# Optimization experiments

Measured on AMD Instinct MI355X. Metric: run time of the kernel, lower is better.

Reference implementation:

```python
import jax, jax.numpy as jnp
import numpy as np

B, S, D, H = 2, 2048, 1024, 16
DK = D // H

def setup_inputs() -> dict:
    key = jax.random.key(0)
    ks = jax.random.split(key, 12)
    def lin(k):
        kw, kb = jax.random.split(k)
        bound = 1.0 / np.sqrt(D)
        W = jax.random.uniform(kw, (D, D), jnp.float32, -bound, bound)
        b = jax.random.uniform(kb, (D,), jnp.float32, -bound, bound)
        return W, b
    Wq, bq = lin(ks[0]); Wk, bk = lin(ks[1]); Wv, bv = lin(ks[2]); Wo, bo = lin(ks[3])
    q = jax.random.normal(ks[4], (B, S, D), jnp.float32)
    k = jax.random.normal(ks[5], (B, S, D), jnp.float32)
    v = jax.random.normal(ks[6], (B, S, D), jnp.float32)
    mask = jnp.ones((1, 1, S, S), jnp.int32)
    return {"q": q, "k": k, "v": v, "mask": mask,
            "Wq": Wq, "bq": bq, "Wk": Wk, "bk": bk,
            "Wv": Wv, "bv": bv, "Wo": Wo, "bo": bo}

def reference(q, k, v, mask, Wq, bq, Wk, bk, Wv, bv, Wo, bo):
    # torch Linear: y = x @ W.T + b
    Q = (q @ Wq.T + bq).reshape(B, S, H, DK).transpose(0, 2, 1, 3)  # [B,H,S,DK]
    K = (k @ Wk.T + bk).reshape(B, S, H, DK).transpose(0, 2, 1, 3)
    V = (v @ Wv.T + bv).reshape(B, S, H, DK).transpose(0, 2, 1, 3)
    scores = jnp.einsum('bhqd,bhkd->bhqk', Q, K) / jnp.sqrt(jnp.float32(DK))
    scores = jnp.where(mask == 0, jnp.float32(-1e9), scores)
    attn = jax.nn.softmax(scores, axis=-1)
    context = jnp.einsum('bhqk,bhkd->bhqd', attn, V)  # [B,H,S,DK]
    concat = context.transpose(0, 2, 1, 3).reshape(B, S, D)
    return concat @ Wo.T + bo
```

## Files before the change

### kernel.cpp

```cpp
#include <hip/hip_runtime.h>
#include <hip/hip_bf16.h>

#define BB 2
#define SS 2048
#define DD 1024
#define HH 16
#define DKK 64

typedef __hip_bfloat16 bf16;
typedef unsigned short u16;
using frag_ab = __attribute__((ext_vector_type(8))) short;
using frag_cd = __attribute__((ext_vector_type(4))) float;

__device__ inline u16 f2bf(float f) {
    bf16 h = __float2bfloat16(f);
    return *reinterpret_cast<u16*>(&h);
}

__device__ inline void gld16(const void* g, void* l) {
    __builtin_amdgcn_global_load_lds((const __attribute__((address_space(1))) void*)g,
                                     (__attribute__((address_space(3))) void*)l,
                                     16, 0, 0);
}

__global__ __launch_bounds__(256) void prep(
    const float* __restrict__ q, const float* __restrict__ k, const float* __restrict__ v,
    const float* __restrict__ Wq, const float* __restrict__ Wk,
    const float* __restrict__ Wv, const float* __restrict__ Wo,
    u16* __restrict__ qb, u16* __restrict__ kb, u16* __restrict__ vb,
    u16* __restrict__ Wqb, u16* __restrict__ Wkb, u16* __restrict__ Wvb, u16* __restrict__ Wob,
    const int* __restrict__ mask, int* __restrict__ flags) {
    int bid = blockIdx.x;
    int t = threadIdx.x;
    if (bid < 8192) {
        const float* src;
        u16* dst;
        int local;
        if (bid < 6144) {
            int ts = bid >> 11;
            local = bid & 2047;
            src = ts == 0 ? q : (ts == 1 ? k : v);
            dst = ts == 0 ? qb : (ts == 1 ? kb : vb);
        } else {
            int wsel = (bid - 6144) >> 9;
            local = (bid - 6144) & 511;
            src = wsel == 0 ? Wq : (wsel == 1 ? Wk : (wsel == 2 ? Wv : Wo));
            dst = wsel == 0 ? Wqb : (wsel == 1 ? Wkb : (wsel == 2 ? Wvb : Wob));
        }
        size_t base = (size_t)local * 2048 + t * 8;
        float4 a = *(const float4*)&src[base];
        float4 b = *(const float4*)&src[base + 4];
        ushort4 u0, u1;
        u0.x = f2bf(a.x); u0.y = f2bf(a.y); u0.z = f2bf(a.z); u0.w = f2bf(a.w);
        u1.x = f2bf(b.x); u1.y = f2bf(b.y); u1.z = f2bf(b.z); u1.w = f2bf(b.w);
        *(ushort4*)&dst[base] = u0;
        *(ushort4*)&dst[base + 4] = u1;
    } else {
        int tile = bid - 8192;
        int qt = tile >> 5, kt = tile & 31;
        __shared__ int f;
        if (t == 0) f = 0;
        __syncthreads();
        int qq = qt * 64 + (t >> 2);
        const int4* row = (const int4*)(mask + (size_t)qq * SS + kt * 64 + (t & 3) * 16);
        int anyz = 0;
#pragma unroll
        for (int i = 0; i < 4; ++i) {
            int4 m4 = row[i];
            anyz |= (m4.x == 0) | (m4.y == 0) | (m4.z == 0) | (m4.w == 0);
        }
        if (anyz) f = 1;
        __syncthreads();
        if (t == 0) flags[tile] = f;
    }
}

__global__ __launch_bounds__(256) void qkv_gemm(
    const u16* __restrict__ Aq, const u16* __restrict__ Ak, const u16* __restrict__ Av,
    const u16* __restrict__ Wq, const u16* __restrict__ Wk, const u16* __restrict__ Wv,
    const float* __restrict__ bq, const float* __restrict__ bk, const float* __restrict__ bv,
    u16* __restrict__ Qo, u16* __restrict__ Ko, u16* __restrict__ Vo) {
    __shared__ u16 As[128 * 32];
    __shared__ u16 Bs[128 * 32];

    int z = blockIdx.z;
    const u16* A = z == 0 ? Aq : (z == 1 ? Ak : Av);
    const u16* W = z == 0 ? Wq : (z == 1 ? Wk : Wv);
    const float* bias = z == 0 ? bq : (z == 1 ? bk : bv);
    u16* out = z == 0 ? Qo : (z == 1 ? Ko : Vo);

    int t = threadIdx.x;
    int m0 = blockIdx.y * 128;
    int n0 = blockIdx.x * 128;
    int w = t >> 6, lane = t & 63;
    int quad = lane >> 4, l16 = lane & 15;
    int wm = w >> 1, wn = w & 1;

    const u16* Ab = A + (size_t)m0 * DD;
    const u16* Wb = W + (size_t)n0 * DD;

    frag_cd acc[4][4];
#pragma unroll
    for (int mt = 0; mt < 4; ++mt)
#pragma unroll
        for (int nt = 0; nt < 4; ++nt) acc[mt][nt] = frag_cd{0.f, 0.f, 0.f, 0.f};

    for (int k0 = 0; k0 < DD; k0 += 32) {
        if (k0) __syncthreads();
#pragma unroll
        for (int i = 0; i < 2; ++i) {
            int c = t + i * 256;
            int row = c >> 2, kc = (c & 3) * 8;
            gld16(Ab + (size_t)row * DD + k0 + kc, &As[c * 8]);
            gld16(Wb + (size_t)row * DD + k0 + kc, &Bs[c * 8]);
        }
        __syncthreads();

        frag_ab af[4], bfr[4];
#pragma unroll
        for (int mt = 0; mt < 4; ++mt)
            af[mt] = *(const frag_ab*)&As[(wm * 64 + mt * 16 + l16) * 32 + quad * 8];
#pragma unroll
        for (int nt = 0; nt < 4; ++nt)
            bfr[nt] = *(const frag_ab*)&Bs[(wn * 64 + nt * 16 + l16) * 32 + quad * 8];
#pragma unroll
        for (int mt = 0; mt < 4; ++mt)
#pragma unroll
            for (int nt = 0; nt < 4; ++nt)
                acc[mt][nt] = __builtin_amdgcn_mfma_f32_16x16x32_bf16(
                    af[mt], bfr[nt], acc[mt][nt], 0, 0, 0);
    }

    float scale = z == 0 ? 0.125f : 1.0f;
#pragma unroll
    for (int nt = 0; nt < 4; ++nt) {
        int n = n0 + wn * 64 + nt * 16 + l16;
        float bv_ = bias[n];
        int h_ = n >> 6, d_ = n & 63;
#pragma unroll
        for (int mt = 0; mt < 4; ++mt) {
            int mb = m0 + wm * 64 + mt * 16 + quad * 4;
            int b_ = mb >> 11, s_ = mb & 2047;
            if (z == 2) {
                ushort4 u;
                u.x = f2bf(acc[mt][nt][0] + bv_);
                u.y = f2bf(acc[mt][nt][1] + bv_);
                u.z = f2bf(acc[mt][nt][2] + bv_);
                u.w = f2bf(acc[mt][nt][3] + bv_);
                *(ushort4*)&out[((size_t)(b_ * HH + h_) * DKK + d_) * SS + s_] = u;
            } else {
#pragma unroll
                for (int r = 0; r < 4; ++r)
                    out[((size_t)(b_ * HH + h_) * SS + s_ + r) * DKK + d_] =
                        f2bf((acc[mt][nt][r] + bv_) * scale);
            }
        }
    }
}

__global__ __launch_bounds__(256) void out_gemm(const u16* __restrict__ A,
                                                const u16* __restrict__ W,
                                                const float* __restrict__ bias,
                                                float* __restrict__ out) {
    __shared__ u16 As[128 * 32];
    __shared__ u16 Bs[128 * 32];

    int t = threadIdx.x;
    int m0 = blockIdx.y * 128;
    int n0 = blockIdx.x * 128;
    int w = t >> 6, lane = t & 63;
    int quad = lane >> 4, l16 = lane & 15;
    int wm = w >> 1, wn = w & 1;

    const u16* Ab = A + (size_t)m0 * DD;
    const u16* Wb = W + (size_t)n0 * DD;

    frag_cd acc[4][4];
#pragma unroll
    for (int mt = 0; mt < 4; ++mt)
#pragma unroll
        for (int nt = 0; nt < 4; ++nt) acc[mt][nt] = frag_cd{0.f, 0.f, 0.f, 0.f};

    for (int k0 = 0; k0 < DD; k0 += 32) {
        if (k0) __syncthreads();
#pragma unroll
        for (int i = 0; i < 2; ++i) {
            int c = t + i * 256;
            int row = c >> 2, kc = (c & 3) * 8;
            gld16(Ab + (size_t)row * DD + k0 + kc, &As[c * 8]);
            gld16(Wb + (size_t)row * DD + k0 + kc, &Bs[c * 8]);
        }
        __syncthreads();

        frag_ab af[4], bfr[4];
#pragma unroll
        for (int mt = 0; mt < 4; ++mt)
            af[mt] = *(const frag_ab*)&As[(wm * 64 + mt * 16 + l16) * 32 + quad * 8];
#pragma unroll
        for (int nt = 0; nt < 4; ++nt)
            bfr[nt] = *(const frag_ab*)&Bs[(wn * 64 + nt * 16 + l16) * 32 + quad * 8];
#pragma unroll
        for (int mt = 0; mt < 4; ++mt)
#pragma unroll
            for (int nt = 0; nt < 4; ++nt)
                acc[mt][nt] = __builtin_amdgcn_mfma_f32_16x16x32_bf16(
                    af[mt], bfr[nt], acc[mt][nt], 0, 0, 0);
    }

#pragma unroll
    for (int nt = 0; nt < 4; ++nt) {
        int n = n0 + wn * 64 + nt * 16 + l16;
        float bv_ = bias[n];
#pragma unroll
        for (int mt = 0; mt < 4; ++mt) {
            int mb = m0 + wm * 64 + mt * 16 + quad * 4;
#pragma unroll
            for (int r = 0; r < 4; ++r)
                out[(size_t)(mb + r) * DD + n] = acc[mt][nt][r] + bv_;
        }
    }
}

__global__ __launch_bounds__(256) void attn_mfma(const u16* __restrict__ Qb,
                                                 const u16* __restrict__ Kb,
                                                 const u16* __restrict__ Vb,
                                                 const int* __restrict__ mask,
                                                 const int* __restrict__ flags,
                                                 u16* __restrict__ C) {
    __shared__ u16 Qs[64 * 64];
    __shared__ u16 Ksb[2][64 * 64];
    __shared__ u16 Vtb[2][64 * 64];
    __shared__ u16 Pw[4][16 * 72];

    int blk = blockIdx.x;
    int qt = blk & 31;
    int bh = blk >> 5;
    int h = bh & 15;
    int b = bh >> 4;
    int q0 = qt * 64;

    const u16* Qg = Qb + ((size_t)bh * SS + q0) * DKK;
    const u16* Kg = Kb + (size_t)bh * SS * DKK;
    const u16* Vg = Vb + (size_t)bh * DKK * SS;
    const int* flg = flags + (qt << 5);

    int t = threadIdx.x;
    int w = t >> 6;
    int lane = t & 63;
    int quad = lane >> 4;
    int l16 = lane & 15;

#pragma unroll
    for (int i = 0; i < 2; ++i) {
        int c = t + i * 256;
        gld16(Qg + c * 8, &Qs[c * 8]);
        gld16(Kg + (size_t)(c >> 3) * DKK + (c & 7) * 8, &Ksb[0][c * 8]);
        gld16(Vg + (size_t)(c >> 3) * SS + (c & 7) * 8, &Vtb[0][c * 8]);
    }
    __syncthreads();

    int qr = w * 16 + l16;
    frag_ab bq0 = *(const frag_ab*)&Qs[qr * 64 + quad * 8];
    frag_ab bq1 = *(const frag_ab*)&Qs[qr * 64 + 32 + quad * 8];

    frag_cd o[4];
#pragma unroll
    for (int dt = 0; dt < 4; ++dt) o[dt] = frag_cd{0.f, 0.f, 0.f, 0.f};
    float m_prev = -1e30f;
    float l_run = 0.f;

    for (int kt = 0; kt < 32; ++kt) {
        const u16* Ks = Ksb[kt & 1];
        const u16* Vt = Vtb[kt & 1];
        if (kt < 31) {
            u16* Kn = Ksb[(kt + 1) & 1];
            u16* Vn = Vtb[(kt + 1) & 1];
#pragma unroll
            for (int i = 0; i < 2; ++i) {
                int c = t + i * 256;
                gld16(Kg + (size_t)((kt + 1) * 64 + (c >> 3)) * DKK + (c & 7) * 8, &Kn[c * 8]);
                gld16(Vg + (size_t)(c >> 3) * SS + (kt + 1) * 64 + (c & 7) * 8, &Vn[c * 8]);
            }
        }
        int anyzero = flg[kt];

        float s[4][4];
#pragma unroll
        for (int nt = 0; nt < 4; ++nt) {
            int kr = nt * 16 + l16;
            frag_ab ak0 = *(const frag_ab*)&Ks[kr * 64 + quad * 8];
            frag_ab ak1 = *(const frag_ab*)&Ks[kr * 64 + 32 + quad * 8];
            frag_cd sf = frag_cd{0.f, 0.f, 0.f, 0.f};
            sf = __builtin_amdgcn_mfma_f32_16x16x32_bf16(ak0, bq0, sf, 0, 0, 0);
            sf = __builtin_amdgcn_mfma_f32_16x16x32_bf16(ak1, bq1, sf, 0, 0, 0);
#pragma unroll
            for (int r = 0; r < 4; ++r) s[nt][r] = sf[r];
        }

        if (anyzero) {
            int qg = q0 + w * 16 + l16;
#pragma unroll
            for (int nt = 0; nt < 4; ++nt)
#pragma unroll
                for (int r = 0; r < 4; ++r) {
                    int kg = kt * 64 + nt * 16 + quad * 4 + r;
                    if (mask[(size_t)qg * SS + kg] == 0) s[nt][r] = -1e9f;
                }
        }

        float mc = s[0][0];
#pragma unroll
        for (int nt = 0; nt < 4; ++nt)
#pragma unroll
            for (int r = 0; r < 4; ++r) mc = fmaxf(mc, s[nt][r]);
        mc = fmaxf(mc, __shfl_xor(mc, 16));
        mc = fmaxf(mc, __shfl_xor(mc, 32));
        float mnew = fmaxf(m_prev, mc);
        float alpha = __expf(m_prev - mnew);

        float p[4][4];
        float ls = 0.f;
#pragma unroll
        for (int nt = 0; nt < 4; ++nt)
#pragma unroll
            for (int r = 0; r < 4; ++r) {
                p[nt][r] = __expf(s[nt][r] - mnew);
                ls += p[nt][r];
            }
        ls += __shfl_xor(ls, 16);
        ls += __shfl_xor(ls, 32);
        l_run = l_run * alpha + ls;
        m_prev = mnew;

#pragma unroll
        for (int dt = 0; dt < 4; ++dt)
#pragma unroll
            for (int r = 0; r < 4; ++r) o[dt][r] *= alpha;

#pragma unroll
        for (int nt = 0; nt < 4; ++nt) {
            ushort4 up;
            up.x = f2bf(p[nt][0]); up.y = f2bf(p[nt][1]);
            up.z = f2bf(p[nt][2]); up.w = f2bf(p[nt][3]);
            *(ushort4*)&Pw[w][l16 * 72 + nt * 16 + quad * 4] = up;
        }
        frag_ab bp0 = *(const frag_ab*)&Pw[w][l16 * 72 + quad * 8];
        frag_ab bp1 = *(const frag_ab*)&Pw[w][l16 * 72 + 32 + quad * 8];

#pragma unroll
        for (int dt = 0; dt < 4; ++dt) {
            int dr = dt * 16 + l16;
            frag_ab av0 = *(const frag_ab*)&Vt[dr * 64 + quad * 8];
            frag_ab av1 = *(const frag_ab*)&Vt[dr * 64 + 32 + quad * 8];
            o[dt] = __builtin_amdgcn_mfma_f32_16x16x32_bf16(av0, bp0, o[dt], 0, 0, 0);
            o[dt] = __builtin_amdgcn_mfma_f32_16x16x32_bf16(av1, bp1, o[dt], 0, 0, 0);
        }
        __syncthreads();
    }

    float inv = 1.f / l_run;
    int qg = q0 + w * 16 + l16;
    u16* Crow = C + ((size_t)b * SS + qg) * DD + h * 64;
#pragma unroll
    for (int dt = 0; dt < 4; ++dt) {
        ushort4 u;
        u.x = f2bf(o[dt][0] * inv);
        u.y = f2bf(o[dt][1] * inv);
        u.z = f2bf(o[dt][2] * inv);
        u.w = f2bf(o[dt][3] * inv);
        *(ushort4*)&Crow[dt * 16 + quad * 4] = u;
    }
}

extern "C" void kernel_launch(void* const* d_in, const int* in_sizes, int n_in,
                              void* d_out, int out_size, void* d_ws, size_t ws_size,
                              hipStream_t stream) {
    const float* q = (const float*)d_in[0];
    const float* k = (const float*)d_in[1];
    const float* v = (const float*)d_in[2];
    const int* mask = (const int*)d_in[3];
    const float* Wq = (const float*)d_in[4];
    const float* bq = (const float*)d_in[5];
    const float* Wk = (const float*)d_in[6];
    const float* bk = (const float*)d_in[7];
    const float* Wv = (const float*)d_in[8];
    const float* bv = (const float*)d_in[9];
    const float* Wo = (const float*)d_in[10];
    const float* bo = (const float*)d_in[11];
    float* out = (float*)d_out;

    const size_t MB = 1024u * 1024u;
    char* ws = (char*)d_ws;
    u16* qb = (u16*)(ws + 0 * MB);
    u16* kb = (u16*)(ws + 8 * MB);
    u16* vb = (u16*)(ws + 16 * MB);
    u16* Wqb = (u16*)(ws + 24 * MB);
    u16* Wkb = (u16*)(ws + 26 * MB);
    u16* Wvb = (u16*)(ws + 28 * MB);
    u16* Wob = (u16*)(ws + 30 * MB);
    u16* Qb = (u16*)(ws + 32 * MB);
    u16* Kb = (u16*)(ws + 40 * MB);
    u16* Vb = (u16*)(ws + 48 * MB);
    int* flags = (int*)(ws + 56 * MB);
    u16* Cw = qb;

    prep<<<9216, 256, 0, stream>>>(q, k, v, Wq, Wk, Wv, Wo,
                                   qb, kb, vb, Wqb, Wkb, Wvb, Wob, mask, flags);

    dim3 grid(DD / 128, (BB * SS) / 128, 3);
    qkv_gemm<<<grid, 256, 0, stream>>>(qb, kb, vb, Wqb, Wkb, Wvb,
                                       bq, bk, bv, Qb, Kb, Vb);

    attn_mfma<<<BB * HH * (SS / 64), 256, 0, stream>>>(Qb, Kb, Vb, mask, flags, Cw);

    out_gemm<<<dim3(DD / 128, (BB * SS) / 128), 256, 0, stream>>>(Cw, Wob, bo, out);
}
```

Measured before the change: 298.8 us.

## Process 128 queries per attention block and prefetch K/V through registers

Each attention block now covers two 64-row query groups, so every K/V tile loaded into shared memory is reused twice. The grid shrinks from 1024 to 512 blocks. Q is read straight from global memory into registers instead of being staged in LDS. The double-buffered async global-to-LDS loads are replaced by register prefetch into a single LDS buffer, with two barriers per iteration. This halves K/V traffic but uses more registers, gives fewer blocks for occupancy, and exposes the LDS store before compute.

```diff
diff --git a/kernel.cpp b/kernel.cpp
--- a/kernel.cpp
+++ b/kernel.cpp
@@ -227,22 +227,19 @@
                                                  const int* __restrict__ mask,
                                                  const int* __restrict__ flags,
                                                  u16* __restrict__ C) {
-    __shared__ u16 Qs[64 * 64];
-    __shared__ u16 Ksb[2][64 * 64];
-    __shared__ u16 Vtb[2][64 * 64];
-    __shared__ u16 Pw[4][16 * 72];
+    __shared__ u16 Ks[64 * 64];
+    __shared__ u16 Vt[64 * 64];
+    __shared__ u16 Pw[4][2][16 * 72];
 
     int blk = blockIdx.x;
-    int qt = blk & 31;
-    int bh = blk >> 5;
+    int Qt = blk & 15;
+    int bh = blk >> 4;
     int h = bh & 15;
     int b = bh >> 4;
-    int q0 = qt * 64;
-
-    const u16* Qg = Qb + ((size_t)bh * SS + q0) * DKK;
+    int q0 = Qt * 128;
+
     const u16* Kg = Kb + (size_t)bh * SS * DKK;
     const u16* Vg = Vb + (size_t)bh * DKK * SS;
-    const int* flg = flags + (qt << 5);
 
     int t = threadIdx.x;
     int w = t >> 6;
@@ -250,125 +247,140 @@
     int quad = lane >> 4;
     int l16 = lane & 15;
 
-#pragma unroll
-    for (int i = 0; i < 2; ++i) {
-        int c = t + i * 256;
-        gld16(Qg + c * 8, &Qs[c * 8]);
-        gld16(Kg + (size_t)(c >> 3) * DKK + (c & 7) * 8, &Ksb[0][c * 8]);
-        gld16(Vg + (size_t)(c >> 3) * SS + (c & 7) * 8, &Vtb[0][c * 8]);
-    }
-    __syncthreads();
-
-    int qr = w * 16 + l16;
-    frag_ab bq0 = *(const frag_ab*)&Qs[qr * 64 + quad * 8];
-    frag_ab bq1 = *(const frag_ab*)&Qs[qr * 64 + 32 + quad * 8];
-
-    frag_cd o[4];
-#pragma unroll
-    for (int dt = 0; dt < 4; ++dt) o[dt] = frag_cd{0.f, 0.f, 0.f, 0.f};
-    float m_prev = -1e30f;
-    float l_run = 0.f;
+    frag_ab bq[2][2];
+#pragma unroll
+    for (int g = 0; g < 2; ++g) {
+        const u16* Qr = Qb + ((size_t)bh * SS + q0 + g * 64 + w * 16 + l16) * DKK;
+        bq[g][0] = *(const frag_ab*)&Qr[quad * 8];
+        bq[g][1] = *(const frag_ab*)&Qr[32 + quad * 8];
+    }
+
+    frag_cd o[2][4];
+#pragma unroll
+    for (int g = 0; g < 2; ++g)
+#pragma unroll
+        for (int dt = 0; dt < 4; ++dt) o[g][dt] = frag_cd{0.f, 0.f, 0.f, 0.f};
+    float m_prev[2] = {-1e30f, -1e30f};
+    float l_run[2] = {0.f, 0.f};
+
+    int vd = t >> 2;
+    int vc = (t & 3) * 16;
+
+    int4 kr0, kr1, vr0, vr1;
+    {
+        const int4* Kt = (const int4*)Kg;
+        kr0 = Kt[2 * t]; kr1 = Kt[2 * t + 1];
+        const int4* Vr = (const int4*)(Vg + (size_t)vd * SS + vc);
+        vr0 = Vr[0]; vr1 = Vr[1];
+    }
 
     for (int kt = 0; kt < 32; ++kt) {
-        const u16* Ks = Ksb[kt & 1];
-        const u16* Vt = Vtb[kt & 1];
+        if (kt) __syncthreads();
+        ((int4*)Ks)[2 * t] = kr0;
+        ((int4*)Ks)[2 * t + 1] = kr1;
+        *(int4*)&Vt[vd * 64 + vc] = vr0;
+        *(int4*)&Vt[vd * 64 + vc + 8] = vr1;
         if (kt < 31) {
-            u16* Kn = Ksb[(kt + 1) & 1];
-            u16* Vn = Vtb[(kt + 1) & 1];
-#pragma unroll
-            for (int i = 0; i < 2; ++i) {
-                int c = t + i * 256;
-                gld16(Kg + (size_t)((kt + 1) * 64 + (c >> 3)) * DKK + (c & 7) * 8, &Kn[c * 8]);
-                gld16(Vg + (size_t)(c >> 3) * SS + (kt + 1) * 64 + (c & 7) * 8, &Vn[c * 8]);
+            const int4* Kt = (const int4*)(Kg + (size_t)(kt + 1) * 4096);
+            kr0 = Kt[2 * t]; kr1 = Kt[2 * t + 1];
+            const int4* Vr = (const int4*)(Vg + (size_t)vd * SS + (kt + 1) * 64 + vc);
+            vr0 = Vr[0]; vr1 = Vr[1];
+        }
+        int az[2];
+        az[0] = flags[(Qt * 2) * 32 + kt];
+        az[1] = flags[(Qt * 2 + 1) * 32 + kt];
+        __syncthreads();
+
+#pragma unroll
+        for (int g = 0; g < 2; ++g) {
+            float s[4][4];
+#pragma unroll
+            for (int nt = 0; nt < 4; ++nt) {
+                int kr = nt * 16 + l16;
+                frag_ab ak0 = *(const frag_ab*)&Ks[kr * 64 + quad * 8];
+                frag_ab ak1 = *(const frag_ab*)&Ks[kr * 64 + 32 + quad * 8];
+                frag_cd sf = frag_cd{0.f, 0.f, 0.f, 0.f};
+                sf = __builtin_amdgcn_mfma_f32_16x16x32_bf16(ak0, bq[g][0], sf, 0, 0, 0);
+                sf = __builtin_amdgcn_mfma_f32_16x16x32_bf16(ak1, bq[g][1], sf, 0, 0, 0);
+#pragma unroll
+                for (int r = 0; r < 4; ++r) s[nt][r] = sf[r];
             }
-        }
-        int anyzero = flg[kt];
-
-        float s[4][4];
-#pragma unroll
-        for (int nt = 0; nt < 4; ++nt) {
-            int kr = nt * 16 + l16;
-            frag_ab ak0 = *(const frag_ab*)&Ks[kr * 64 + quad * 8];
-            frag_ab ak1 = *(const frag_ab*)&Ks[kr * 64 + 32 + quad * 8];
-            frag_cd sf = frag_cd{0.f, 0.f, 0.f, 0.f};
-            sf = __builtin_amdgcn_mfma_f32_16x16x32_bf16(ak0, bq0, sf, 0, 0, 0);
-            sf = __builtin_amdgcn_mfma_f32_16x16x32_bf16(ak1, bq1, sf, 0, 0, 0);
-#pragma unroll
-            for (int r = 0; r < 4; ++r) s[nt][r] = sf[r];
-        }
-
-        if (anyzero) {
-            int qg = q0 + w * 16 + l16;
+
+            if (az[g]) {
+                int qg = q0 + g * 64 + w * 16 + l16;
+#pragma unroll
+                for (int nt = 0; nt < 4; ++nt)
+#pragma unroll
+                    for (int r = 0; r < 4; ++r) {
+                        int kg = kt * 64 + nt * 16 + quad * 4 + r;
+                        if (mask[(size_t)qg * SS + kg] == 0) s[nt][r] = -1e9f;
+                    }
+            }
+
+            float mc = s[0][0];
 #pragma unroll
             for (int nt = 0; nt < 4; ++nt)
 #pragma unroll
+                for (int r = 0; r < 4; ++r) mc = fmaxf(mc, s[nt][r]);
+            mc = fmaxf(mc, __shfl_xor(mc, 16));
+            mc = fmaxf(mc, __shfl_xor(mc, 32));
+            float mnew = fmaxf(m_prev[g], mc);
+            float alpha = __expf(m_prev[g] - mnew);
+
+            float p[4][4];
+            float ls = 0.f;
+#pragma unroll
+            for (int nt = 0; nt < 4; ++nt)
+#pragma unroll
                 for (int r = 0; r < 4; ++r) {
-                    int kg = kt * 64 + nt * 16 + quad * 4 + r;
-                    if (mask[(size_t)qg * SS + kg] == 0) s[nt][r] = -1e9f;
+                    p[nt][r] = __expf(s[nt][r] - mnew);
+                    ls += p[nt][r];
                 }
-        }
-
-        float mc = s[0][0];
-#pragma unroll
-        for (int nt = 0; nt < 4; ++nt)
-#pragma unroll
-            for (int r = 0; r < 4; ++r) mc = fmaxf(mc, s[nt][r]);
-        mc = fmaxf(mc, __shfl_xor(mc, 16));
-        mc = fmaxf(mc, __shfl_xor(mc, 32));
-        float mnew = fmaxf(m_prev, mc);
-        float alpha = __expf(m_prev - mnew);
-
-        float p[4][4];
-        float ls = 0.f;
-#pragma unroll
-        for (int nt = 0; nt < 4; ++nt)
-#pragma unroll
-            for (int r = 0; r < 4; ++r) {
-                p[nt][r] = __expf(s[nt][r] - mnew);
-                ls += p[nt][r];
+            ls += __shfl_xor(ls, 16);
+            ls += __shfl_xor(ls, 32);
+            l_run[g] = l_run[g] * alpha + ls;
+            m_prev[g] = mnew;
+
+#pragma unroll
+            for (int dt = 0; dt < 4; ++dt)
+#pragma unroll
+                for (int r = 0; r < 4; ++r) o[g][dt][r] *= alpha;
+
+#pragma unroll
+            for (int nt = 0; nt < 4; ++nt) {
+                ushort4 up;
+                up.x = f2bf(p[nt][0]); up.y = f2bf(p[nt][1]);
+                up.z = f2bf(p[nt][2]); up.w = f2bf(p[nt][3]);
+                *(ushort4*)&Pw[w][g][l16 * 72 + nt * 16 + quad * 4] = up;
             }
-        ls += __shfl_xor(ls, 16);
-        ls += __shfl_xor(ls, 32);
-        l_run = l_run * alpha + ls;
-        m_prev = mnew;
-
-#pragma unroll
-        for (int dt = 0; dt < 4; ++dt)
-#pragma unroll
-            for (int r = 0; r < 4; ++r) o[dt][r] *= alpha;
-
-#pragma unroll
-        for (int nt = 0; nt < 4; ++nt) {
-            ushort4 up;
-            up.x = f2bf(p[nt][0]); up.y = f2bf(p[nt][1]);
-            up.z = f2bf(p[nt][2]); up.w = f2bf(p[nt][3]);
-            *(ushort4*)&Pw[w][l16 * 72 + nt * 16 + quad * 4] = up;
-        }
-        frag_ab bp0 = *(const frag_ab*)&Pw[w][l16 * 72 + quad * 8];
-        frag_ab bp1 = *(const frag_ab*)&Pw[w][l16 * 72 + 32 + quad * 8];
-
+            frag_ab bp0 = *(const frag_ab*)&Pw[w][g][l16 * 72 + quad * 8];
+            frag_ab bp1 = *(const frag_ab*)&Pw[w][g][l16 * 72 + 32 + quad * 8];
+
+#pragma unroll
+            for (int dt = 0; dt < 4; ++dt) {
+                int dr = dt * 16 + l16;
+                frag_ab av0 = *(const frag_ab*)&Vt[dr * 64 + quad * 8];
+                frag_ab av1 = *(const frag_ab*)&Vt[dr * 64 + 32 + quad * 8];
+                o[g][dt] = __builtin_amdgcn_mfma_f32_16x16x32_bf16(av0, bp0, o[g][dt], 0, 0, 0);
+                o[g][dt] = __builtin_amdgcn_mfma_f32_16x16x32_bf16(av1, bp1, o[g][dt], 0, 0, 0);
+            }
+        }
+    }
+
+#pragma unroll
+    for (int g = 0; g < 2; ++g) {
+        float inv = 1.f / l_run[g];
+        int qg = q0 + g * 64 + w * 16 + l16;
+        u16* Crow = C + ((size_t)b * SS + qg) * DD + h * 64;
 #pragma unroll
         for (int dt = 0; dt < 4; ++dt) {
-            int dr = dt * 16 + l16;
-            frag_ab av0 = *(const frag_ab*)&Vt[dr * 64 + quad * 8];
-            frag_ab av1 = *(const frag_ab*)&Vt[dr * 64 + 32 + quad * 8];
-            o[dt] = __builtin_amdgcn_mfma_f32_16x16x32_bf16(av0, bp0, o[dt], 0, 0, 0);
-            o[dt] = __builtin_amdgcn_mfma_f32_16x16x32_bf16(av1, bp1, o[dt], 0, 0, 0);
-        }
-        __syncthreads();
-    }
-
-    float inv = 1.f / l_run;
-    int qg = q0 + w * 16 + l16;
-    u16* Crow = C + ((size_t)b * SS + qg) * DD + h * 64;
-#pragma unroll
-    for (int dt = 0; dt < 4; ++dt) {
-        ushort4 u;
-        u.x = f2bf(o[dt][0] * inv);
-        u.y = f2bf(o[dt][1] * inv);
-        u.z = f2bf(o[dt][2] * inv);
-        u.w = f2bf(o[dt][3] * inv);
-        *(ushort4*)&Crow[dt * 16 + quad * 4] = u;
+            ushort4 u;
+            u.x = f2bf(o[g][dt][0] * inv);
+            u.y = f2bf(o[g][dt][1] * inv);
+            u.z = f2bf(o[g][dt][2] * inv);
+            u.w = f2bf(o[g][dt][3] * inv);
+            *(ushort4*)&Crow[dt * 16 + quad * 4] = u;
+        }
     }
 }
 
@@ -411,7 +423,7 @@
     qkv_gemm<<<grid, 256, 0, stream>>>(qb, kb, vb, Wqb, Wkb, Wvb,
                                        bq, bk, bv, Qb, Kb, Vb);
 
-    attn_mfma<<<BB * HH * (SS / 64), 256, 0, stream>>>(Qb, Kb, Vb, mask, flags, Cw);
+    attn_mfma<<<BB * HH * (SS / 128), 256, 0, stream>>>(Qb, Kb, Vb, mask, flags, Cw);
 
     out_gemm<<<dim3(DD / 128, (BB * SS) / 128), 256, 0, stream>>>(Cw, Wob, bo, out);
 }
```

After: 291.2 us. 2.5% less time.
